# Optimization experiments

Measured on AMD Instinct MI355X. Metric: run time of the kernel, lower is better.

## Reference

```python
import jax, jax.numpy as jnp
import numpy as np

B, T, N, HOR = 64, 12, 1024, 12
D_IN, D_OUT, RNN, E, K = 1, 1, 64, 8, 3
MEM_N, MEM_D = 10, 32
DEC = RNN + MEM_D  # 96 (memory_type='local')
YCOV = 1


def setup_inputs() -> dict:
    key = jax.random.key(0)
    ks = jax.random.split(key, 12)
    s = 0.1  # xavier-ish scale for weights
    return {
        "x": jax.random.normal(ks[0], (B, T, N, D_IN), jnp.float32),
        "y_cov": jax.random.normal(ks[1], (B, HOR, N, YCOV), jnp.float32),
        "node_embeddings": jax.random.normal(ks[2], (N, E), jnp.float32),
        "enc_gate_W": jax.random.normal(ks[3], (K * (D_IN + RNN), 2 * RNN), jnp.float32) * s,
        "enc_gate_b": jnp.zeros((2 * RNN,), jnp.float32),
        "enc_up_W": jax.random.normal(ks[4], (K * (D_IN + RNN), RNN), jnp.float32) * s,
        "enc_up_b": jnp.zeros((RNN,), jnp.float32),
        "Memory": jax.random.normal(ks[5], (MEM_N, MEM_D), jnp.float32) * s,
        "Wq": jax.random.normal(ks[6], (RNN, MEM_D), jnp.float32) * s,
        "FC_E": jax.random.normal(ks[7], (MEM_D, E), jnp.float32) * s,
        "dec_gate_W": jax.random.normal(ks[8], (K * (D_OUT + YCOV + DEC), 2 * DEC), jnp.float32) * s,
        "dec_gate_b": jnp.zeros((2 * DEC,), jnp.float32),
        "dec_up_W": jax.random.normal(ks[9], (K * (D_OUT + YCOV + DEC), DEC), jnp.float32) * s,
        "dec_up_b": jnp.zeros((DEC,), jnp.float32),
        "proj_W": jax.random.normal(ks[10], (DEC, D_OUT), jnp.float32) * s,
        "proj_b": jnp.zeros((D_OUT,), jnp.float32),
    }


def _cheb_supports(S):
    # S: (N,N) soft adjacency -> stacked Chebyshev set [I, S, 2S@S_{k-1}-S_{k-2}, ...], (K,N,N)
    n = S.shape[0]
    sup = [jnp.eye(n, dtype=S.dtype), S]
    for _ in range(2, K):
        sup.append(2.0 * S @ sup[-1] - sup[-2])
    return jnp.stack(sup)


def _agcn(xin, supports, W, b):
    # xin: (B,N,C); supports: (K,N,N); W: (K*C, O)
    xg = jnp.einsum('knm,bmc->bnkc', supports, xin)  # k-major matches torch cat order
    bsz, n = xin.shape[0], xin.shape[1]
    xg = xg.reshape(bsz, n, -1)
    return xg @ W + b


def _cell(xt, state, supports, gW, gb, uW, ub, hdim):
    inp = jnp.concatenate([xt, state], axis=-1)
    z_r = jax.nn.sigmoid(_agcn(inp, supports, gW, gb))
    z, r = z_r[..., :hdim], z_r[..., hdim:]
    cand = jnp.concatenate([xt, z * state], axis=-1)
    hc = jnp.tanh(_agcn(cand, supports, uW, ub))
    return r * state + (1.0 - r) * hc


def reference(x, y_cov, node_embeddings, enc_gate_W, enc_gate_b, enc_up_W, enc_up_b,
              Memory, Wq, FC_E, dec_gate_W, dec_gate_b, dec_up_W, dec_up_b, proj_W, proj_b):
    # ---- encoder supports from static node embeddings (2D path in AGCN) ----
    S_enc = jax.nn.softmax(jax.nn.relu(node_embeddings @ node_embeddings.T), axis=1)
    sup_enc = _cheb_supports(S_enc)

    # ---- encoder: GRU-style recurrence over T timesteps (lax.scan) ----
    def enc_step(state, xt):
        h = _cell(xt, state, sup_enc, enc_gate_W, enc_gate_b, enc_up_W, enc_up_b, RNN)
        return h, None
    h0 = jnp.zeros((x.shape[0], N, RNN), x.dtype)
    h_t, _ = jax.lax.scan(enc_step, h0, jnp.swapaxes(x, 0, 1))  # final hidden (B,N,RNN)

    # ---- memory query (memory_type='local') ----
    query = h_t @ Wq                                  # (B,N,MEM_D)
    att = jax.nn.softmax(query @ Memory.T, axis=-1)   # (B,N,MEM_N)
    proto_t = att @ Memory                            # (B,N,MEM_D)
    W_E = proto_t @ FC_E                              # (B,N,E) meta node embeddings

    # ---- decoder supports from meta embeddings (3D path: einsum sums over batch) ----
    S_dec = jax.nn.softmax(jax.nn.relu(jnp.einsum('bnc,bmc->nm', W_E, W_E)), axis=1)
    sup_dec = _cheb_supports(S_dec)

    # ---- stepwise decoder with go symbol ----
    dec_h0 = jnp.concatenate([h_t, proto_t], axis=-1)  # (B,N,DEC)
    go0 = jnp.zeros((x.shape[0], N, D_OUT), x.dtype)

    def dec_step(carry, yc_t):
        go, state = carry
        xt = jnp.concatenate([go, yc_t], axis=-1)
        h = _cell(xt, state, sup_dec, dec_gate_W, dec_gate_b, dec_up_W, dec_up_b, DEC)
        go_new = h @ proj_W + proj_b
        return (go_new, h), go_new

    _, outs = jax.lax.scan(dec_step, (go0, dec_h0), jnp.swapaxes(y_cov, 0, 1))
    return jnp.swapaxes(outs, 0, 1)  # (B, horizon, N, D_OUT)
```

## Files before the change

### kernel.cpp

```cpp
#include <hip/hip_runtime.h>
#include <hip/hip_bf16.h>

constexpr int B_ = 64, T_ = 12, NN = 1024, HOR_ = 12;

typedef __attribute__((ext_vector_type(8))) short short8;
typedef __attribute__((ext_vector_type(4))) float f32x4;
typedef unsigned short ushort_t;

static __device__ inline ushort_t f2bh(float v) {
  __hip_bfloat16 h = __float2bfloat16(v);
  return *reinterpret_cast<ushort_t*>(&h);
}
static __device__ inline float bh2f(ushort_t u) {
  __hip_bfloat16 h = *reinterpret_cast<__hip_bfloat16*>(&u);
  return __bfloat162float(h);
}
static __device__ inline void split_bf16(float v, ushort_t& hi, ushort_t& lo) {
  hi = f2bh(v);
  lo = f2bh(v - bh2f(hi));
}

static __device__ inline void gload_lds16(const ushort_t* g, ushort_t* l) {
  __builtin_amdgcn_global_load_lds(
      (const __attribute__((address_space(1))) unsigned int*)g,
      (__attribute__((address_space(3))) unsigned int*)l, 16, 0, 0);
}

__global__ void gemm_nt_kernel(const float* __restrict__ A, const float* __restrict__ Bm,
                               float* __restrict__ C, int Ncol, int Kd) {
  __shared__ float As[16][68];
  __shared__ float Bs[16][68];
  const int bm = blockIdx.y * 64, bn = blockIdx.x * 64;
  const int tid = threadIdx.x;
  const int tx = tid & 15, ty = tid >> 4;
  float acc[4][4] = {};
  for (int k0 = 0; k0 < Kd; k0 += 16) {
#pragma unroll
    for (int r = 0; r < 4; ++r) {
      const int m = (tid >> 4) + r * 16;
      const int kk = tid & 15;
      const int k = k0 + kk;
      As[kk][m] = (k < Kd) ? A[(size_t)(bm + m) * Kd + k] : 0.f;
      Bs[kk][m] = (k < Kd) ? Bm[(size_t)(bn + m) * Kd + k] : 0.f;
    }
    __syncthreads();
#pragma unroll
    for (int kk = 0; kk < 16; ++kk) {
      float a[4], b[4];
#pragma unroll
      for (int i = 0; i < 4; ++i) a[i] = As[kk][ty * 4 + i];
#pragma unroll
      for (int j = 0; j < 4; ++j) b[j] = Bs[kk][tx * 4 + j];
#pragma unroll
      for (int i = 0; i < 4; ++i)
#pragma unroll
        for (int j = 0; j < 4; ++j) acc[i][j] += a[i] * b[j];
    }
    __syncthreads();
  }
#pragma unroll
  for (int i = 0; i < 4; ++i)
#pragma unroll
    for (int j = 0; j < 4; ++j)
      C[(size_t)(bm + ty * 4 + i) * Ncol + bn + tx * 4 + j] = acc[i][j];
}

__global__ void relu_softmax_kernel(float* __restrict__ S, ushort_t* __restrict__ Sh,
                                    ushort_t* __restrict__ Sl) {
  const int row = blockIdx.x;
  float* r = S + (size_t)row * NN;
  const int tid = threadIdx.x;
  float v[4];
  float mx = 0.f;
#pragma unroll
  for (int j = 0; j < 4; ++j) {
    float xv = fmaxf(r[tid + j * 256], 0.f);
    v[j] = xv;
    mx = fmaxf(mx, xv);
  }
#pragma unroll
  for (int off = 1; off < 64; off <<= 1) mx = fmaxf(mx, __shfl_xor(mx, off));
  __shared__ float sred[4];
  const int wv = tid >> 6;
  if ((tid & 63) == 0) sred[wv] = mx;
  __syncthreads();
  mx = fmaxf(fmaxf(sred[0], sred[1]), fmaxf(sred[2], sred[3]));
  __syncthreads();
  float s = 0.f;
#pragma unroll
  for (int j = 0; j < 4; ++j) { v[j] = expf(v[j] - mx); s += v[j]; }
#pragma unroll
  for (int off = 1; off < 64; off <<= 1) s += __shfl_xor(s, off);
  if ((tid & 63) == 0) sred[wv] = s;
  __syncthreads();
  s = sred[0] + sred[1] + sred[2] + sred[3];
  const float inv = 1.f / s;
#pragma unroll
  for (int j = 0; j < 4; ++j) {
    const float sv = v[j] * inv;
    const size_t e = (size_t)row * NN + tid + j * 256;
    r[tid + j * 256] = sv;
    ushort_t hi, lo;
    split_bf16(sv, hi, lo);
    Sh[e] = hi;
    Sl[e] = lo;
  }
}

__global__ void st_kernel(const float* __restrict__ S, ushort_t* __restrict__ STh,
                          ushort_t* __restrict__ STl) {
  __shared__ float tile[64][65];
  const int bx = blockIdx.x * 64, by = blockIdx.y * 64;
  const int tid = threadIdx.x;
  const int cl = tid & 63, rq = tid >> 6;
#pragma unroll
  for (int r = 0; r < 16; ++r) {
    const int rr = rq + r * 4;
    tile[rr][cl] = S[(size_t)(by + rr) * NN + bx + cl];
  }
  __syncthreads();
#pragma unroll
  for (int r = 0; r < 16; ++r) {
    const int rr = rq + r * 4;
    const float v = tile[cl][rr];
    ushort_t hi, lo;
    split_bf16(v, hi, lo);
    STh[(size_t)(bx + rr) * NN + by + cl] = hi;
    STl[(size_t)(bx + rr) * NN + by + cl] = lo;
  }
}

__global__ void cheb_mfma_kernel(const ushort_t* __restrict__ S1h,
                                 const ushort_t* __restrict__ S1l,
                                 const ushort_t* __restrict__ STh,
                                 const ushort_t* __restrict__ STl,
                                 ushort_t* __restrict__ Mh) {
  __shared__ __align__(16) ushort_t sA[2 * 32 * 64];
  __shared__ __align__(16) ushort_t sB[2 * 64 * 64];
  const int bj = blockIdx.x * 64, bn = blockIdx.y * 32;
  const int tid = threadIdx.x;
  const int w = tid >> 6, lane = tid & 63;
  const int row = lane & 15, kq = lane >> 4;
  const int srow8 = lane >> 3, sslot = lane & 7;
  f32x4 acc[2] = {};
  for (int k0 = 0; k0 < NN; k0 += 64) {
#pragma unroll
    for (int t2 = 0; t2 < 2; ++t2) {
      const int c = w + t2 * 4, p = c >> 2, i = c & 3;
      const int grow = i * 8 + srow8;
      const int gch = sslot ^ (grow & 7);
      const ushort_t* src = (p ? S1l : S1h) + (size_t)(bn + grow) * NN + k0 + gch * 8;
      gload_lds16(src, sA + p * 2048 + i * 512);
    }
#pragma unroll
    for (int t2 = 0; t2 < 4; ++t2) {
      const int c2 = w + t2 * 4, p = c2 >> 3, rb = c2 & 7;
      const int grow = rb * 8 + srow8;
      const int gch = sslot ^ (grow & 7);
      const ushort_t* src = (p ? STl : STh) + (size_t)(bj + grow) * NN + k0 + gch * 8;
      gload_lds16(src, sB + p * 4096 + rb * 512);
    }
    __syncthreads();
#pragma unroll
    for (int kk = 0; kk < 2; ++kk) {
      const int rB = w * 16 + row;
      const int chB = ((kk * 4 + kq) ^ (rB & 7)) * 8;
      const short8 bh = *(const short8*)(sB + rB * 64 + chB);
      const short8 bl = *(const short8*)(sB + 4096 + rB * 64 + chB);
#pragma unroll
      for (int mt = 0; mt < 2; ++mt) {
        const int rA = mt * 16 + row;
        const int chA = ((kk * 4 + kq) ^ (rA & 7)) * 8;
        const short8 ah = *(const short8*)(sA + rA * 64 + chA);
        const short8 al = *(const short8*)(sA + 2048 + rA * 64 + chA);
        acc[mt] = __builtin_amdgcn_mfma_f32_16x16x32_bf16(ah, bh, acc[mt], 0, 0, 0);
        acc[mt] = __builtin_amdgcn_mfma_f32_16x16x32_bf16(ah, bl, acc[mt], 0, 0, 0);
        acc[mt] = __builtin_amdgcn_mfma_f32_16x16x32_bf16(al, bh, acc[mt], 0, 0, 0);
      }
    }
    __syncthreads();
  }
  const int j = bj + w * 16 + row;
#pragma unroll
  for (int mt = 0; mt < 2; ++mt) {
    const int node0 = bn + mt * 16 + kq * 4;
#pragma unroll
    for (int r = 0; r < 4; ++r)
      Mh[(size_t)(node0 + r) * NN + j] = f2bh(2.f * acc[mt][r]);
  }
}

__global__ void wt_kernel(const float* __restrict__ W, ushort_t* __restrict__ Wth,
                          int KK, int NO, int KP, int NOP) {
  const int e = blockIdx.x * 256 + threadIdx.x;
  if (e >= NOP * KP) return;
  const int no = e / KP, k = e - no * KP;
  const float v = (no < NO && k < KK) ? W[(size_t)k * NO + no] : 0.f;
  Wth[e] = f2bh(v);
}

template <int C, int KP, int MODE>
__global__ void prep_kernel(const float* __restrict__ src0, const float* __restrict__ src1,
                            const float* __restrict__ hst, const float* __restrict__ zr,
                            ushort_t* __restrict__ Agh, ushort_t* __restrict__ XTh, int t) {
  __shared__ float tile[64][65];
  const int bj = blockIdx.x * 64, bn = blockIdx.y * 64;
  const int tid = threadIdx.x;
  const int jl = tid & 63, nq = tid >> 6;
  const int j = bj + jl;
  const int b = j / C, c = j - b * C;
#pragma unroll
  for (int r = 0; r < 16; ++r) {
    const int node = bn + nq + r * 4;
    const int idx = node * 64 + b;
    float v;
    if (MODE == 0) {
      v = (c == 0) ? src0[((size_t)b * T_ + t) * NN + node]
                   : hst[(size_t)idx * 64 + (c - 1)];
    } else if (MODE == 1) {
      v = (c == 0) ? src0[((size_t)b * T_ + t) * NN + node]
                   : zr[(size_t)idx * 128 + (c - 1)] * hst[(size_t)idx * 64 + (c - 1)];
    } else if (MODE == 2) {
      v = (c == 0) ? src0[idx]
        : (c == 1) ? src1[((size_t)b * HOR_ + t) * NN + node]
                   : hst[(size_t)idx * 96 + (c - 2)];
    } else {
      v = (c == 0) ? src0[idx]
        : (c == 1) ? src1[((size_t)b * HOR_ + t) * NN + node]
                   : zr[(size_t)idx * 192 + (c - 2)] * hst[(size_t)idx * 96 + (c - 2)];
    }
    tile[nq + r * 4][jl] = v;
    Agh[(size_t)idx * KP + c] = f2bh(v);
  }
  __syncthreads();
  const int nl = tid & 63, jq = tid >> 6;
#pragma unroll
  for (int r = 0; r < 16; ++r) {
    const int jj = bj + jq + r * 4;
    XTh[(size_t)jj * NN + bn + nl] = f2bh(tile[nl][jq + r * 4]);
  }
}

template <int C, int KP>
__global__ void graph_mfma_kernel(const ushort_t* __restrict__ S1h,
                                  const ushort_t* __restrict__ Mh,
                                  const ushort_t* __restrict__ XTh,
                                  ushort_t* __restrict__ Agh) {
  constexpr int W = B_ * C;
  const int bj = blockIdx.x * 128;
  if (bj >= W) return;
  __shared__ __align__(16) ushort_t sA[2 * 32 * 64];
  __shared__ __align__(16) ushort_t sB[128 * 64];
  const int bn = blockIdx.y * 32;
  const int tid = threadIdx.x;
  const int w = tid >> 6, lane = tid & 63;
  const int row = lane & 15, kq = lane >> 4;
  const int srow8 = lane >> 3;
  const int sslot = lane & 7;

  const int s = w >> 1;
  const int jhalf = (w & 1) * 64;
  const ushort_t* A_lds = sA + s * (32 * 64);

  f32x4 acc[2][4] = {};
  for (int k0 = 0; k0 < NN; k0 += 64) {
#pragma unroll
    for (int t2 = 0; t2 < 6; ++t2) {
      const int cid = w + t2 * 4;
      if (cid < 8) {
        const int p = cid >> 2, i = cid & 3;
        const int grow = i * 8 + srow8;
        const int gch = sslot ^ (grow & 7);
        const ushort_t* g = (p ? Mh : S1h) + (size_t)(bn + grow) * NN + k0 + gch * 8;
        gload_lds16(g, sA + p * (32 * 64) + i * 512);
      } else {
        const int rb = cid - 8;
        const int brow = rb * 8 + srow8;
        const int gch = sslot ^ (brow & 7);
        const ushort_t* g = XTh + (size_t)(bj + brow) * NN + k0 + gch * 8;
        gload_lds16(g, sB + rb * 512);
      }
    }
    __syncthreads();
    short8 a[2][2];
#pragma unroll
    for (int kk = 0; kk < 2; ++kk)
#pragma unroll
      for (int mt = 0; mt < 2; ++mt) {
        const int r = mt * 16 + row;
        const int chunk = (kk * 4 + kq) ^ (r & 7);
        a[kk][mt] = *(const short8*)(A_lds + r * 64 + chunk * 8);
      }
#pragma unroll
    for (int nt = 0; nt < 4; ++nt) {
#pragma unroll
      for (int kk = 0; kk < 2; ++kk) {
        const int r = jhalf + nt * 16 + row;
        const int chunk = (kk * 4 + kq) ^ (r & 7);
        const short8 bh = *(const short8*)(sB + r * 64 + chunk * 8);
#pragma unroll
        for (int mt = 0; mt < 2; ++mt)
          acc[mt][nt] = __builtin_amdgcn_mfma_f32_16x16x32_bf16(a[kk][mt], bh, acc[mt][nt], 0, 0, 0);
      }
    }
    __syncthreads();
  }
  const int slice_off = (s + 1) * C;
#pragma unroll
  for (int nt = 0; nt < 4; ++nt) {
    const int j = bj + jhalf + nt * 16 + row;
    if (j < W) {
      const int b = j / C, c = j - b * C;
      const size_t coloff = (size_t)(slice_off + c);
#pragma unroll
      for (int mt = 0; mt < 2; ++mt) {
        const int node0 = bn + mt * 16 + kq * 4;
        float sub[4] = {0.f, 0.f, 0.f, 0.f};
        if (s == 1) {
          const ushort_t* xp = XTh + (size_t)j * NN + node0;
#pragma unroll
          for (int r = 0; r < 4; ++r) sub[r] = bh2f(xp[r]);
        }
#pragma unroll
        for (int r = 0; r < 4; ++r) {
          const size_t a = (size_t)((node0 + r) * 64 + b) * KP + coloff;
          Agh[a] = f2bh(acc[mt][nt][r] - sub[r]);
        }
      }
    }
  }
}

template <int KP, int NO, int NOP, int MODE, int H>
__global__ void dense_mfma_kernel(const ushort_t* __restrict__ Agh,
                                  const ushort_t* __restrict__ Wth,
                                  const float* __restrict__ bias,
                                  float* __restrict__ outp,
                                  const float* __restrict__ zrin) {
  constexpr int NFR = NO / 16;
  __shared__ __align__(16) ushort_t sAh[128 * 32];
  __shared__ __align__(16) ushort_t sBh[NOP * 32];
  const int row0 = blockIdx.x * 128;
  const int tid = threadIdx.x;
  const int w = tid >> 6, lane = tid & 63;
  const int col16 = lane & 15, four = lane >> 4;
  const int srow = lane >> 2;
  const int scol = ((lane & 3) ^ ((srow >> 1) & 3)) * 8;
  const int kqs = (four ^ ((col16 >> 1) & 3)) * 8;
  f32x4 acc[2][NFR] = {};
  for (int k0 = 0; k0 < KP; k0 += 32) {
    for (int c = w; c < 8; c += 4) {
      const size_t g = (size_t)(row0 + c * 16 + srow) * KP + k0 + scol;
      gload_lds16(Agh + g, sAh + c * 512);
    }
    for (int c = w; c < NOP / 16; c += 4) {
      const size_t g = (size_t)(c * 16 + srow) * KP + k0 + scol;
      gload_lds16(Wth + g, sBh + c * 512);
    }
    __syncthreads();
    short8 ah[2];
#pragma unroll
    for (int mt = 0; mt < 2; ++mt) {
      const int r = (w * 32 + mt * 16 + col16) * 32 + kqs;
      ah[mt] = *(const short8*)(sAh + r);
    }
#pragma unroll
    for (int nt = 0; nt < NFR; ++nt) {
      const int r = (nt * 16 + col16) * 32 + kqs;
      const short8 bh = *(const short8*)(sBh + r);
#pragma unroll
      for (int mt = 0; mt < 2; ++mt)
        acc[mt][nt] = __builtin_amdgcn_mfma_f32_16x16x32_bf16(ah[mt], bh, acc[mt][nt], 0, 0, 0);
    }
    __syncthreads();
  }
#pragma unroll
  for (int nt = 0; nt < NFR; ++nt) {
    const int col = nt * 16 + col16;
    const float bv = bias[col];
#pragma unroll
    for (int mt = 0; mt < 2; ++mt) {
      const int rbase = row0 + w * 32 + mt * 16 + four * 4;
#pragma unroll
      for (int r = 0; r < 4; ++r) {
        const int row = rbase + r;
        const float v = acc[mt][nt][r] + bv;
        if (MODE == 0) {
          outp[(size_t)row * NO + col] = 1.f / (1.f + expf(-v));
        } else {
          const float rg = zrin[(size_t)row * (2 * H) + H + col];
          const float hv = outp[(size_t)row * H + col];
          outp[(size_t)row * H + col] = rg * hv + (1.f - rg) * tanhf(v);
        }
      }
    }
  }
}

__global__ void attn_kernel(const float* __restrict__ h, const float* __restrict__ Wq,
                            const float* __restrict__ Mem, const float* __restrict__ FCE,
                            float* __restrict__ hB, float* __restrict__ WE) {
  __shared__ float sWq[64 * 32];
  __shared__ float sM[10 * 32];
  __shared__ float sF[32 * 8];
  const int tid = threadIdx.x;
  for (int i = tid; i < 64 * 32; i += 256) sWq[i] = Wq[i];
  for (int i = tid; i < 10 * 32; i += 256) sM[i] = Mem[i];
  for (int i = tid; i < 32 * 8; i += 256) sF[i] = FCE[i];
  __syncthreads();
  const int idx = blockIdx.x * 256 + tid;
  const float* hp = h + (size_t)idx * 64;
  float* hd = hB + (size_t)idx * 96;
  float q[32] = {};
  for (int i0 = 0; i0 < 16; ++i0) {
    const float4 h4 = *(const float4*)(hp + i0 * 4);
#pragma unroll
    for (int jj = 0; jj < 4; ++jj) {
      const float hv = ((const float*)&h4)[jj];
      hd[i0 * 4 + jj] = hv;
      const int i = i0 * 4 + jj;
#pragma unroll
      for (int c = 0; c < 32; ++c) q[c] += hv * sWq[i * 32 + c];
    }
  }
  float lg[10];
  float mx = -1e30f;
#pragma unroll
  for (int m = 0; m < 10; ++m) {
    float s = 0.f;
#pragma unroll
    for (int c = 0; c < 32; ++c) s += q[c] * sM[m * 32 + c];
    lg[m] = s;
    mx = fmaxf(mx, s);
  }
  float den = 0.f;
#pragma unroll
  for (int m = 0; m < 10; ++m) { lg[m] = expf(lg[m] - mx); den += lg[m]; }
  const float inv = 1.f / den;
  float p[32] = {};
#pragma unroll
  for (int m = 0; m < 10; ++m) {
    const float a = lg[m] * inv;
#pragma unroll
    for (int c = 0; c < 32; ++c) p[c] += a * sM[m * 32 + c];
  }
#pragma unroll
  for (int c = 0; c < 32; ++c) hd[64 + c] = p[c];
  float* wd = WE + (size_t)idx * 8;
#pragma unroll
  for (int e = 0; e < 8; ++e) {
    float s = 0.f;
#pragma unroll
    for (int c = 0; c < 32; ++c) s += p[c] * sF[c * 8 + e];
    wd[e] = s;
  }
}

__global__ void proj_kernel(const float* __restrict__ h, const float* __restrict__ pW,
                            const float* __restrict__ pb, float* __restrict__ go,
                            float* __restrict__ out, int t) {
  __shared__ float sW[96];
  if (threadIdx.x < 96) sW[threadIdx.x] = pW[threadIdx.x];
  __syncthreads();
  const int idx = blockIdx.x * 256 + threadIdx.x;
  const float* hp = h + (size_t)idx * 96;
  float acc = pb[0];
  for (int j0 = 0; j0 < 24; ++j0) {
    const float4 h4 = *(const float4*)(hp + j0 * 4);
    acc += h4.x * sW[j0 * 4] + h4.y * sW[j0 * 4 + 1] + h4.z * sW[j0 * 4 + 2] + h4.w * sW[j0 * 4 + 3];
  }
  go[idx] = acc;
  const int n = idx >> 6, b = idx & 63;
  out[((size_t)b * HOR_ + t) * NN + n] = acc;
}

extern "C" void kernel_launch(void* const* d_in, const int* in_sizes, int n_in,
                              void* d_out, int out_size, void* d_ws, size_t ws_size,
                              hipStream_t stream) {
  const float* x    = (const float*)d_in[0];
  const float* ycov = (const float*)d_in[1];
  const float* emb  = (const float*)d_in[2];
  const float* egW  = (const float*)d_in[3];
  const float* egb  = (const float*)d_in[4];
  const float* euW  = (const float*)d_in[5];
  const float* eub  = (const float*)d_in[6];
  const float* Mem  = (const float*)d_in[7];
  const float* Wq   = (const float*)d_in[8];
  const float* FCE  = (const float*)d_in[9];
  const float* dgW  = (const float*)d_in[10];
  const float* dgb  = (const float*)d_in[11];
  const float* duW  = (const float*)d_in[12];
  const float* dub  = (const float*)d_in[13];
  const float* pW   = (const float*)d_in[14];
  const float* pb   = (const float*)d_in[15];
  float* out = (float*)d_out;

  char* w = (char*)d_ws;
  auto alloc = [&](size_t bytes) {
    void* p = (void*)w;
    w += (bytes + 255) & ~(size_t)255;
    return p;
  };
  float* S1  = (float*)alloc((size_t)NN * NN * 4);
  float* zr  = (float*)alloc((size_t)NN * B_ * 192 * 4);
  float* hA  = (float*)alloc((size_t)NN * B_ * 64 * 4);
  float* hB  = (float*)alloc((size_t)NN * B_ * 96 * 4);
  float* go  = (float*)alloc((size_t)NN * B_ * 4);
  float* WE  = (float*)alloc((size_t)NN * B_ * 8 * 4);
  ushort_t* S1h = (ushort_t*)alloc((size_t)NN * NN * 2);
  ushort_t* S1l = (ushort_t*)alloc((size_t)NN * NN * 2);
  ushort_t* Mh  = (ushort_t*)alloc((size_t)NN * NN * 2);
  ushort_t* STh = (ushort_t*)alloc((size_t)NN * NN * 2);
  ushort_t* STl = (ushort_t*)alloc((size_t)NN * NN * 2);
  ushort_t* XTh = (ushort_t*)alloc((size_t)B_ * 98 * NN * 2);
  ushort_t* Agh = (ushort_t*)alloc((size_t)NN * B_ * 320 * 2);
  ushort_t* WtegH = (ushort_t*)alloc(128 * 224 * 2);
  ushort_t* WteuH = (ushort_t*)alloc(64 * 224 * 2);
  ushort_t* WtdgH = (ushort_t*)alloc(192 * 320 * 2);
  ushort_t* WtduH = (ushort_t*)alloc(128 * 320 * 2);
  (void)ws_size; (void)in_sizes; (void)n_in; (void)out_size;

  const dim3 blk(256);

  wt_kernel<<<(128 * 224 + 255) / 256, blk, 0, stream>>>(egW, WtegH, 195, 128, 224, 128);
  wt_kernel<<<(64 * 224 + 255) / 256, blk, 0, stream>>>(euW, WteuH, 195, 64, 224, 64);
  wt_kernel<<<(192 * 320 + 255) / 256, blk, 0, stream>>>(dgW, WtdgH, 294, 192, 320, 192);
  wt_kernel<<<(128 * 320 + 255) / 256, blk, 0, stream>>>(duW, WtduH, 294, 96, 320, 128);
  hipMemsetAsync(Agh, 0, (size_t)NN * B_ * 320 * 2, stream);
  hipMemsetAsync(hA, 0, (size_t)NN * B_ * 64 * 4, stream);
  hipMemsetAsync(go, 0, (size_t)NN * B_ * 4, stream);

  gemm_nt_kernel<<<dim3(16, 16), blk, 0, stream>>>(emb, emb, S1, NN, 8);
  relu_softmax_kernel<<<NN, blk, 0, stream>>>(S1, S1h, S1l);
  st_kernel<<<dim3(16, 16), blk, 0, stream>>>(S1, STh, STl);
  cheb_mfma_kernel<<<dim3(16, 32), blk, 0, stream>>>(S1h, S1l, STh, STl, Mh);

  for (int t = 0; t < T_; ++t) {
    prep_kernel<65, 224, 0><<<dim3(65, 16), blk, 0, stream>>>(x, nullptr, hA, nullptr, Agh, XTh, t);
    graph_mfma_kernel<65, 224><<<dim3(40, 32), blk, 0, stream>>>(S1h, Mh, XTh, Agh);
    dense_mfma_kernel<224, 128, 128, 0, 64><<<512, blk, 0, stream>>>(Agh, WtegH, egb, zr, nullptr);
    prep_kernel<65, 224, 1><<<dim3(65, 16), blk, 0, stream>>>(x, nullptr, hA, zr, Agh, XTh, t);
    graph_mfma_kernel<65, 224><<<dim3(40, 32), blk, 0, stream>>>(S1h, Mh, XTh, Agh);
    dense_mfma_kernel<224, 64, 64, 1, 64><<<512, blk, 0, stream>>>(Agh, WteuH, eub, hA, zr);
  }

  attn_kernel<<<256, blk, 0, stream>>>(hA, Wq, Mem, FCE, hB, WE);
  gemm_nt_kernel<<<dim3(16, 16), blk, 0, stream>>>(WE, WE, S1, NN, 512);
  relu_softmax_kernel<<<NN, blk, 0, stream>>>(S1, S1h, S1l);
  st_kernel<<<dim3(16, 16), blk, 0, stream>>>(S1, STh, STl);
  cheb_mfma_kernel<<<dim3(16, 32), blk, 0, stream>>>(S1h, S1l, STh, STl, Mh);

  for (int t = 0; t < HOR_; ++t) {
    prep_kernel<98, 320, 2><<<dim3(98, 16), blk, 0, stream>>>(go, ycov, hB, nullptr, Agh, XTh, t);
    graph_mfma_kernel<98, 320><<<dim3(56, 32), blk, 0, stream>>>(S1h, Mh, XTh, Agh);
    dense_mfma_kernel<320, 192, 192, 0, 96><<<512, blk, 0, stream>>>(Agh, WtdgH, dgb, zr, nullptr);
    prep_kernel<98, 320, 3><<<dim3(98, 16), blk, 0, stream>>>(go, ycov, hB, zr, Agh, XTh, t);
    graph_mfma_kernel<98, 320><<<dim3(56, 32), blk, 0, stream>>>(S1h, Mh, XTh, Agh);
    dense_mfma_kernel<320, 96, 128, 1, 96><<<512, blk, 0, stream>>>(Agh, WtduH, dub, hB, zr);
    proj_kernel<<<256, blk, 0, stream>>>(hB, pW, pb, go, out, t);
  }
}
```

Before: 3.860 ms.

## Fuse gate epilogues into writing bf16 GCN inputs directly, replacing prep with transpose

The dense gate kernel's epilogue now computes z*h and writes it as bf16 straight into the aggregation input buffer. It stores only the r gate in a smaller fp32 buffer instead of the full z/r tensor. The update epilogue likewise writes the new hidden state into that buffer, and proj writes the next go and y_cov columns. The per-step prep kernels become a bf16-to-bf16 transpose, plus a tiny x-column writer in the encoder. This removes fp32 reads of zr and h and redundant conversions, in exchange for cross-kernel coupling and scattered bf16 stores in the epilogues.

```diff
diff --git a/kernel.cpp b/kernel.cpp
--- a/kernel.cpp
+++ b/kernel.cpp
@@ -201,8 +201,8 @@
 
 template <int C, int KP, int MODE>
 __global__ void prep_kernel(const float* __restrict__ src0, const float* __restrict__ src1,
-                            const float* __restrict__ hst, const float* __restrict__ zr,
-                            ushort_t* __restrict__ Agh, ushort_t* __restrict__ XTh, int t) {
+                            const float* __restrict__ hst,
+                            ushort_t* __restrict__ Agh, ushort_t* __restrict__ XTh) {
   __shared__ float tile[64][65];
   const int bj = blockIdx.x * 64, bn = blockIdx.y * 64;
   const int tid = threadIdx.x;
@@ -215,19 +215,12 @@
     const int idx = node * 64 + b;
     float v;
     if (MODE == 0) {
-      v = (c == 0) ? src0[((size_t)b * T_ + t) * NN + node]
+      v = (c == 0) ? src0[((size_t)b * T_) * NN + node]
                    : hst[(size_t)idx * 64 + (c - 1)];
-    } else if (MODE == 1) {
-      v = (c == 0) ? src0[((size_t)b * T_ + t) * NN + node]
-                   : zr[(size_t)idx * 128 + (c - 1)] * hst[(size_t)idx * 64 + (c - 1)];
-    } else if (MODE == 2) {
-      v = (c == 0) ? src0[idx]
-        : (c == 1) ? src1[((size_t)b * HOR_ + t) * NN + node]
-                   : hst[(size_t)idx * 96 + (c - 2)];
     } else {
       v = (c == 0) ? src0[idx]
-        : (c == 1) ? src1[((size_t)b * HOR_ + t) * NN + node]
-                   : zr[(size_t)idx * 192 + (c - 2)] * hst[(size_t)idx * 96 + (c - 2)];
+        : (c == 1) ? src1[((size_t)b * HOR_) * NN + node]
+                   : hst[(size_t)idx * 96 + (c - 2)];
     }
     tile[nq + r * 4][jl] = v;
     Agh[(size_t)idx * KP + c] = f2bh(v);
@@ -239,6 +232,34 @@
     const int jj = bj + jq + r * 4;
     XTh[(size_t)jj * NN + bn + nl] = f2bh(tile[nl][jq + r * 4]);
   }
+}
+
+template <int C, int KP>
+__global__ void xt_kernel(const ushort_t* __restrict__ Agh, ushort_t* __restrict__ XTh) {
+  __shared__ ushort_t tile[64][70];
+  const int bj = blockIdx.x * 64, bn = blockIdx.y * 64;
+  const int tid = threadIdx.x;
+  const int jl = tid & 63, nq = tid >> 6;
+  const int j = bj + jl;
+  const int b = j / C, c = j - b * C;
+#pragma unroll
+  for (int r = 0; r < 16; ++r) {
+    const int node = bn + nq + r * 4;
+    tile[nq + r * 4][jl] = Agh[(size_t)(node * 64 + b) * KP + c];
+  }
+  __syncthreads();
+  const int nl = tid & 63, jq = tid >> 6;
+#pragma unroll
+  for (int r = 0; r < 16; ++r) {
+    const int jj = bj + jq + r * 4;
+    XTh[(size_t)jj * NN + bn + nl] = tile[nl][jq + r * 4];
+  }
+}
+
+__global__ void set_x_kernel(const float* __restrict__ x, ushort_t* __restrict__ Agh, int t) {
+  const int idx = blockIdx.x * 256 + threadIdx.x;
+  const int n = idx >> 6, b = idx & 63;
+  Agh[(size_t)idx * 224] = f2bh(x[((size_t)b * T_ + t) * NN + n]);
 }
 
 template <int C, int KP>
@@ -331,12 +352,12 @@
   }
 }
 
-template <int KP, int NO, int NOP, int MODE, int H>
-__global__ void dense_mfma_kernel(const ushort_t* __restrict__ Agh,
+template <int KP, int NO, int NOP, int MODE, int H, int CO>
+__global__ void dense_mfma_kernel(ushort_t* __restrict__ Agh,
                                   const ushort_t* __restrict__ Wth,
                                   const float* __restrict__ bias,
-                                  float* __restrict__ outp,
-                                  const float* __restrict__ zrin) {
+                                  float* __restrict__ hstate,
+                                  float* __restrict__ rbuf) {
   constexpr int NFR = NO / 16;
   __shared__ __align__(16) ushort_t sAh[128 * 32];
   __shared__ __align__(16) ushort_t sBh[NOP * 32];
@@ -385,12 +406,20 @@
       for (int r = 0; r < 4; ++r) {
         const int row = rbase + r;
         const float v = acc[mt][nt][r] + bv;
-        if (MODE == 0) {
-          outp[(size_t)row * NO + col] = 1.f / (1.f + expf(-v));
+        if (MODE == 2) {
+          const float sg = 1.f / (1.f + expf(-v));
+          if (col < H) {
+            const float hv = hstate[(size_t)row * H + col];
+            Agh[(size_t)row * KP + CO + col] = f2bh(sg * hv);
+          } else {
+            rbuf[(size_t)row * H + (col - H)] = sg;
+          }
         } else {
-          const float rg = zrin[(size_t)row * (2 * H) + H + col];
-          const float hv = outp[(size_t)row * H + col];
-          outp[(size_t)row * H + col] = rg * hv + (1.f - rg) * tanhf(v);
+          const float rg = rbuf[(size_t)row * H + col];
+          const float hv = hstate[(size_t)row * H + col];
+          const float hnew = rg * hv + (1.f - rg) * tanhf(v);
+          hstate[(size_t)row * H + col] = hnew;
+          Agh[(size_t)row * KP + CO + col] = f2bh(hnew);
         }
       }
     }
@@ -458,6 +487,7 @@
 
 __global__ void proj_kernel(const float* __restrict__ h, const float* __restrict__ pW,
                             const float* __restrict__ pb, float* __restrict__ go,
+                            const float* __restrict__ ycov, ushort_t* __restrict__ Agh,
                             float* __restrict__ out, int t) {
   __shared__ float sW[96];
   if (threadIdx.x < 96) sW[threadIdx.x] = pW[threadIdx.x];
@@ -472,6 +502,10 @@
   go[idx] = acc;
   const int n = idx >> 6, b = idx & 63;
   out[((size_t)b * HOR_ + t) * NN + n] = acc;
+  if (t + 1 < HOR_) {
+    Agh[(size_t)idx * 320 + 0] = f2bh(acc);
+    Agh[(size_t)idx * 320 + 1] = f2bh(ycov[((size_t)b * HOR_ + t + 1) * NN + n]);
+  }
 }
 
 extern "C" void kernel_launch(void* const* d_in, const int* in_sizes, int n_in,
@@ -501,12 +535,12 @@
     w += (bytes + 255) & ~(size_t)255;
     return p;
   };
-  float* S1  = (float*)alloc((size_t)NN * NN * 4);
-  float* zr  = (float*)alloc((size_t)NN * B_ * 192 * 4);
-  float* hA  = (float*)alloc((size_t)NN * B_ * 64 * 4);
-  float* hB  = (float*)alloc((size_t)NN * B_ * 96 * 4);
-  float* go  = (float*)alloc((size_t)NN * B_ * 4);
-  float* WE  = (float*)alloc((size_t)NN * B_ * 8 * 4);
+  float* S1   = (float*)alloc((size_t)NN * NN * 4);
+  float* rbuf = (float*)alloc((size_t)NN * B_ * 96 * 4);
+  float* hA   = (float*)alloc((size_t)NN * B_ * 64 * 4);
+  float* hB   = (float*)alloc((size_t)NN * B_ * 96 * 4);
+  float* go   = (float*)alloc((size_t)NN * B_ * 4);
+  float* WE   = (float*)alloc((size_t)NN * B_ * 8 * 4);
   ushort_t* S1h = (ushort_t*)alloc((size_t)NN * NN * 2);
   ushort_t* S1l = (ushort_t*)alloc((size_t)NN * NN * 2);
   ushort_t* Mh  = (ushort_t*)alloc((size_t)NN * NN * 2);
@@ -536,12 +570,17 @@
   cheb_mfma_kernel<<<dim3(16, 32), blk, 0, stream>>>(S1h, S1l, STh, STl, Mh);
 
   for (int t = 0; t < T_; ++t) {
-    prep_kernel<65, 224, 0><<<dim3(65, 16), blk, 0, stream>>>(x, nullptr, hA, nullptr, Agh, XTh, t);
+    if (t == 0) {
+      prep_kernel<65, 224, 0><<<dim3(65, 16), blk, 0, stream>>>(x, nullptr, hA, Agh, XTh);
+    } else {
+      set_x_kernel<<<256, blk, 0, stream>>>(x, Agh, t);
+      xt_kernel<65, 224><<<dim3(65, 16), blk, 0, stream>>>(Agh, XTh);
+    }
     graph_mfma_kernel<65, 224><<<dim3(40, 32), blk, 0, stream>>>(S1h, Mh, XTh, Agh);
-    dense_mfma_kernel<224, 128, 128, 0, 64><<<512, blk, 0, stream>>>(Agh, WtegH, egb, zr, nullptr);
-    prep_kernel<65, 224, 1><<<dim3(65, 16), blk, 0, stream>>>(x, nullptr, hA, zr, Agh, XTh, t);
+    dense_mfma_kernel<224, 128, 128, 2, 64, 1><<<512, blk, 0, stream>>>(Agh, WtegH, egb, hA, rbuf);
+    xt_kernel<65, 224><<<dim3(65, 16), blk, 0, stream>>>(Agh, XTh);
     graph_mfma_kernel<65, 224><<<dim3(40, 32), blk, 0, stream>>>(S1h, Mh, XTh, Agh);
-    dense_mfma_kernel<224, 64, 64, 1, 64><<<512, blk, 0, stream>>>(Agh, WteuH, eub, hA, zr);
+    dense_mfma_kernel<224, 64, 64, 1, 64, 1><<<512, blk, 0, stream>>>(Agh, WteuH, eub, hA, rbuf);
   }
 
   attn_kernel<<<256, blk, 0, stream>>>(hA, Wq, Mem, FCE, hB, WE);
@@ -551,12 +590,16 @@
   cheb_mfma_kernel<<<dim3(16, 32), blk, 0, stream>>>(S1h, S1l, STh, STl, Mh);
 
   for (int t = 0; t < HOR_; ++t) {
-    prep_kernel<98, 320, 2><<<dim3(98, 16), blk, 0, stream>>>(go, ycov, hB, nullptr, Agh, XTh, t);
+    if (t == 0) {
+      prep_kernel<98, 320, 2><<<dim3(98, 16), blk, 0, stream>>>(go, ycov, hB, Agh, XTh);
+    } else {
+      xt_kernel<98, 320><<<dim3(98, 16), blk, 0, stream>>>(Agh, XTh);
+    }
     graph_mfma_kernel<98, 320><<<dim3(56, 32), blk, 0, stream>>>(S1h, Mh, XTh, Agh);
-    dense_mfma_kernel<320, 192, 192, 0, 96><<<512, blk, 0, stream>>>(Agh, WtdgH, dgb, zr, nullptr);
-    prep_kernel<98, 320, 3><<<dim3(98, 16), blk, 0, stream>>>(go, ycov, hB, zr, Agh, XTh, t);
+    dense_mfma_kernel<320, 192, 192, 2, 96, 2><<<512, blk, 0, stream>>>(Agh, WtdgH, dgb, hB, rbuf);
+    xt_kernel<98, 320><<<dim3(98, 16), blk, 0, stream>>>(Agh, XTh);
     graph_mfma_kernel<98, 320><<<dim3(56, 32), blk, 0, stream>>>(S1h, Mh, XTh, Agh);
-    dense_mfma_kernel<320, 96, 128, 1, 96><<<512, blk, 0, stream>>>(Agh, WtduH, dub, hB, zr);
-    proj_kernel<<<256, blk, 0, stream>>>(hB, pW, pb, go, out, t);
-  }
-}
+    dense_mfma_kernel<320, 96, 128, 1, 96, 2><<<512, blk, 0, stream>>>(Agh, WtduH, dub, hB, rbuf);
+    proj_kernel<<<256, blk, 0, stream>>>(hB, pW, pb, go, ycov, Agh, out, t);
+  }
+}
```

New measurement: 3.893 ms. No clear change (+0.9%).
